# Performance work log

Measured on AMD Instinct MI355X. Metric: run time of the kernel, lower is better.

## Reference

```python
import jax, jax.numpy as jnp
import numpy as np

HIDDEN = 2048
INNER = 1024
NUM_EXPERTS = 64
TOP_K = 8
T_TOKENS = 512


def setup_inputs() -> dict:
    key = jax.random.key(0)
    k_x, k_gw, k_gb, k_w1, k_w2 = jax.random.split(key, 5)
    x = jax.random.normal(k_x, (T_TOKENS, HIDDEN), dtype=jnp.float32)
    gate_w = jax.random.normal(k_gw, (NUM_EXPERTS, HIDDEN), dtype=jnp.float32) * 0.02
    gate_b = jax.random.normal(k_gb, (NUM_EXPERTS,), dtype=jnp.float32) * 0.02
    # fc1: fused gate+up, [E, 2*INNER, HIDDEN]; fc2: down, [E, HIDDEN, INNER]
    w1 = jax.random.normal(k_w1, (NUM_EXPERTS, 2 * INNER, HIDDEN), dtype=jnp.float32) * 0.02
    w2 = jax.random.normal(k_w2, (NUM_EXPERTS, HIDDEN, INNER), dtype=jnp.float32) * 0.02
    return {"x": x, "gate_w": gate_w, "gate_b": gate_b, "w1": w1, "w2": w2}


def reference(x, gate_w, gate_b, w1, w2):
    # Router: ReplicatedLinear with bias -> logits [T, E]
    logits = x @ gate_w.T + gate_b
    # FusedMoE default routing: softmax (fp32), top-k, renormalize
    probs = jax.nn.softmax(logits.astype(jnp.float32), axis=-1)
    topk_w, topk_idx = jax.lax.top_k(probs, TOP_K)          # [T, K]
    topk_w = topk_w / jnp.sum(topk_w, axis=-1, keepdims=True)
    T, E = probs.shape
    # Sparse combine weights scattered into a dense [T, E] matrix
    combine = jnp.zeros((T, E), dtype=topk_w.dtype)
    combine = combine.at[jnp.arange(T)[:, None], topk_idx].add(topk_w)
    # Expert MLPs (dense-over-experts reference; combine zeros out unrouted pairs)
    h = jnp.einsum('th,eih->tei', x, w1)                    # [T, E, 2*INNER]
    gate_h, up_h = h[..., :INNER], h[..., INNER:]
    act = jax.nn.gelu(gate_h, approximate=True) * up_h      # gelu_pytorch_tanh
    y = jnp.einsum('tei,ehi->teh', act, w2)                 # [T, E, HIDDEN]
    # Weighted scatter-combine back to tokens
    return jnp.einsum('te,teh->th', combine.astype(x.dtype), y)
```

## Files before the change

### kernel.cpp

```cpp
#include <hip/hip_runtime.h>
#include <hip/hip_bf16.h>

#define HIDDEN 2048
#define INNER  1024
#define NE     64
#define TOPK   8
#define NTOK   512

typedef float f32x4 __attribute__((ext_vector_type(4)));
typedef short bf16x8 __attribute__((ext_vector_type(8)));

static __device__ __forceinline__ unsigned short b16(float f) {
  return __builtin_bit_cast(unsigned short, __float2bfloat16(f));
}
static __device__ __forceinline__ unsigned int pk2(float lo, float hi) {
  return (unsigned)b16(lo) | ((unsigned)b16(hi) << 16);
}

static __device__ __forceinline__ void decode_ce32(int flat, int& c, int& e) {
  int xcd = flat & 7, s = flat >> 3;
  c = s & 31;
  e = ((s >> 5) << 3) | xcd;
}

__global__ __launch_bounds__(256) void gating_kernel(
    const float* __restrict__ x, const float* __restrict__ gw, const float* __restrict__ gb,
    int* __restrict__ ticket, int* __restrict__ counts, int* __restrict__ offsets,
    int* __restrict__ topk_e, float* __restrict__ topk_w,
    int* __restrict__ perm_tok, int* __restrict__ invpos,
    unsigned short* __restrict__ xb) {
  const int t = blockIdx.x;
  const int tid = threadIdx.x;
  const int lane = tid & 63, w = tid >> 6;

  {
    const float4* xi = (const float4*)(x + (size_t)t * HIDDEN);
    float4 v0 = xi[tid * 2], v1 = xi[tid * 2 + 1];
    ushort4 o0, o1;
    o0.x = b16(v0.x); o0.y = b16(v0.y); o0.z = b16(v0.z); o0.w = b16(v0.w);
    o1.x = b16(v1.x); o1.y = b16(v1.y); o1.z = b16(v1.z); o1.w = b16(v1.w);
    ushort4* xo = (ushort4*)(xb + (size_t)t * HIDDEN);
    xo[tid * 2] = o0; xo[tid * 2 + 1] = o1;
  }

  const int e = tid >> 2, seg = tid & 3;
  const f32x4* gr = (const f32x4*)(gw + (size_t)e * HIDDEN);
  const f32x4* xr = (const f32x4*)(x + (size_t)t * HIDDEN);
  float acc = 0.f;
  #pragma unroll 8
  for (int k = 0; k < 128; ++k) {
    int idx = k * 4 + seg;
    f32x4 a = xr[idx], b = gr[idx];
    acc += a.x * b.x + a.y * b.y + a.z * b.z + a.w * b.w;
  }
  acc += __shfl_xor(acc, 1);
  acc += __shfl_xor(acc, 2);
  __shared__ float sP[NE];
  if (seg == 0) sP[e] = acc;
  __syncthreads();

  __shared__ float sW[TOPK];
  __shared__ int   sE[TOPK];
  if (w == 0) {
    float logit = gb[lane] + sP[lane];
    float m = logit;
    #pragma unroll
    for (int off = 32; off; off >>= 1) m = fmaxf(m, __shfl_xor(m, off));
    float p = __expf(logit - m);
    float s = p;
    #pragma unroll
    for (int off = 32; off; off >>= 1) s += __shfl_xor(s, off);
    p /= s;
    float myp = p;
    #pragma unroll
    for (int k = 0; k < TOPK; ++k) {
      float v = myp; int ei = lane;
      #pragma unroll
      for (int off = 32; off; off >>= 1) {
        float v2 = __shfl_xor(v, off); int e2 = __shfl_xor(ei, off);
        if (v2 > v || (v2 == v && e2 < ei)) { v = v2; ei = e2; }
      }
      if (lane == 0) { sW[k] = v; sE[k] = ei; }
      if (lane == ei) myp = -1.0f;
    }
  }
  __syncthreads();
  if (tid < TOPK) {
    float ss = 0.f;
    #pragma unroll
    for (int k = 0; k < TOPK; ++k) ss += sW[k];
    topk_e[t * TOPK + tid] = sE[tid];
    topk_w[t * TOPK + tid] = sW[tid] / ss;
  }

  __threadfence();
  __syncthreads();
  __shared__ int slast;
  if (tid == 0) {
    int old = atomicAdd(ticket, 1);
    slast = (old == (int)gridDim.x - 1);
  }
  __syncthreads();
  if (!slast) return;
  __threadfence();

  __shared__ int hcnt[NE], soff[NE], ccur[NE];
  if (tid < NE) hcnt[tid] = 0;
  __syncthreads();
  for (int i = tid; i < NTOK * TOPK; i += 256) atomicAdd(&hcnt[topk_e[i]], 1);
  __syncthreads();
  if (tid < NE) {
    int c = hcnt[tid];
    int s = c;
    #pragma unroll
    for (int off = 1; off < 64; off <<= 1) {
      int o = __shfl_up(s, off);
      if (tid >= off) s += o;
    }
    soff[tid] = s - c; ccur[tid] = 0;
    counts[tid] = c; offsets[tid] = s - c;
  }
  __syncthreads();
  for (int i = tid; i < NTOK * TOPK; i += 256) {
    int ee = topk_e[i];
    int p = atomicAdd(&ccur[ee], 1);
    int pos = soff[ee] + p;
    perm_tok[pos] = i >> 3;
    invpos[i] = pos;
  }
}

__global__ __launch_bounds__(256, 3) void phase1_kernel(
    const unsigned short* __restrict__ xb, const float* __restrict__ w1,
    const int* __restrict__ offsets, const int* __restrict__ counts,
    const int* __restrict__ perm_tok, unsigned short* __restrict__ act) {
  int c, e;
  decode_ce32(blockIdx.x, c, e);
  const int n_e = counts[e];
  if (n_e == 0) return;
  const int off = offsets[e];
  const int tid = threadIdx.x;
  const int lane = tid & 63, wave = tid >> 6;
  const int u2 = lane >> 4, l15 = lane & 15;
  const int mat = wave >> 1;
  const int wm  = (wave & 1) * 64;

  const int r16 = tid >> 4, l16 = tid & 15;
  const float* wg  = w1 + (size_t)e * (2 * INNER) * HIDDEN;
  const float* rp0 = wg + (size_t)(c * 32 + r16) * HIDDEN;
  const float* rp1 = rp0 + (size_t)16 * HIDDEN;
  const float* rp2 = wg + (size_t)(INNER + c * 32 + r16) * HIDDEN;
  const float* rp3 = rp2 + (size_t)16 * HIDDEN;
  const int bidx0 = r16 * 16 + (((l16 >> 1) ^ (r16 & 7)) << 1) + (l16 & 1);

  const int ar = tid >> 3, as = tid & 7;
  const int sxa = as ^ (ar & 7);

  __shared__ uint4 smem[2][1536];
  __shared__ int stok[128];
  float (*sU)[36] = (float(*)[36])&smem[0][0];

  for (int m0 = 0; m0 < n_e; m0 += 128) {
    __syncthreads();
    if (tid < 128) {
      int idx = m0 + tid;
      stok[tid] = perm_tok[off + (idx < n_e ? idx : n_e - 1)];
    }
    __syncthreads();

    const unsigned short* xr0 = xb + (size_t)stok[ar] * HIDDEN;
    const unsigned short* xr1 = xb + (size_t)stok[ar + 32] * HIDDEN;
    const unsigned short* xr2 = xb + (size_t)stok[ar + 64] * HIDDEN;
    const unsigned short* xr3 = xb + (size_t)stok[ar + 96] * HIDDEN;

    uint4 va0 = *((const uint4*)xr0 + as);
    uint4 va1 = *((const uint4*)xr1 + as);
    uint4 va2 = *((const uint4*)xr2 + as);
    uint4 va3 = *((const uint4*)xr3 + as);
    f32x4 vB0 = *((const f32x4*)rp0 + l16);
    f32x4 vB1 = *((const f32x4*)rp1 + l16);
    f32x4 vB2 = *((const f32x4*)rp2 + l16);
    f32x4 vB3 = *((const f32x4*)rp3 + l16);

    f32x4 acc[4][2];
    #pragma unroll
    for (int i = 0; i < 4; ++i)
      #pragma unroll
      for (int j = 0; j < 2; ++j) acc[i][j] = (f32x4)0.f;

    for (int k0 = 0; k0 < HIDDEN; k0 += 64) {
      const int cur = (k0 >> 6) & 1;
      uint4* A = smem[cur];
      A[ar * 8 + sxa]          = va0;
      A[(ar + 32) * 8 + sxa]   = va1;
      A[(ar + 64) * 8 + sxa]   = va2;
      A[(ar + 96) * 8 + sxa]   = va3;
      {
        uint2* bb = (uint2*)(smem[cur] + 1024);
        bb[bidx0]       = make_uint2(pk2(vB0.x, vB0.y), pk2(vB0.z, vB0.w));
        bb[bidx0 + 256] = make_uint2(pk2(vB1.x, vB1.y), pk2(vB1.z, vB1.w));
        bb[bidx0 + 512] = make_uint2(pk2(vB2.x, vB2.y), pk2(vB2.z, vB2.w));
        bb[bidx0 + 768] = make_uint2(pk2(vB3.x, vB3.y), pk2(vB3.z, vB3.w));
      }
      __syncthreads();
      int k1 = k0 + 64;
      if (k1 < HIDDEN) {
        va0 = *((const uint4*)(xr0 + k1) + as);
        va1 = *((const uint4*)(xr1 + k1) + as);
        va2 = *((const uint4*)(xr2 + k1) + as);
        va3 = *((const uint4*)(xr3 + k1) + as);
        vB0 = *((const f32x4*)(rp0 + k1) + l16);
        vB1 = *((const f32x4*)(rp1 + k1) + l16);
        vB2 = *((const f32x4*)(rp2 + k1) + l16);
        vB3 = *((const f32x4*)(rp3 + k1) + l16);
      }
      const uint4* Bq = smem[cur] + 1024;
      #pragma unroll
      for (int ks = 0; ks < 2; ++ks) {
        const int u = ks * 4 + u2;
        bf16x8 af[4], bfr[2];
        #pragma unroll
        for (int mi = 0; mi < 4; ++mi) {
          int r = wm + mi * 16 + l15;
          af[mi] = __builtin_bit_cast(bf16x8, A[r * 8 + (u ^ (r & 7))]);
        }
        #pragma unroll
        for (int ni = 0; ni < 2; ++ni) {
          int r = mat * 32 + ni * 16 + l15;
          bfr[ni] = __builtin_bit_cast(bf16x8, Bq[r * 8 + (u ^ (r & 7))]);
        }
        #pragma unroll
        for (int mi = 0; mi < 4; ++mi)
          #pragma unroll
          for (int ni = 0; ni < 2; ++ni)
            acc[mi][ni] = __builtin_amdgcn_mfma_f32_16x16x32_bf16(af[mi], bfr[ni], acc[mi][ni], 0, 0, 0);
      }
    }

    __syncthreads();
    if (mat == 1) {
      #pragma unroll
      for (int mi = 0; mi < 4; ++mi)
        #pragma unroll
        for (int ni = 0; ni < 2; ++ni)
          #pragma unroll
          for (int r4 = 0; r4 < 4; ++r4)
            sU[wm + mi * 16 + u2 * 4 + r4][ni * 16 + l15] = acc[mi][ni][r4];
    }
    __syncthreads();
    if (mat == 0) {
      #pragma unroll
      for (int mi = 0; mi < 4; ++mi)
        #pragma unroll
        for (int r4 = 0; r4 < 4; ++r4) {
          int mrow = wm + mi * 16 + u2 * 4 + r4;
          int m = m0 + mrow;
          if (m < n_e) {
            unsigned short* arow = act + (size_t)(off + m) * INNER + c * 32;
            #pragma unroll
            for (int ni = 0; ni < 2; ++ni) {
              int col = ni * 16 + l15;
              float g = acc[mi][ni][r4];
              float uu = sU[mrow][col];
              float ge = g / (1.0f + __expf(-1.5957691216057308f * (g + 0.044715f * g * g * g)));
              arow[col] = b16(ge * uu);
            }
          }
        }
    }
  }
}

__global__ __launch_bounds__(256, 3) void phase2_kernel(
    const unsigned short* __restrict__ act, const float* __restrict__ w2,
    const int* __restrict__ offsets, const int* __restrict__ counts,
    float* __restrict__ ybuf) {
  int c, e;
  decode_ce32(blockIdx.x, c, e);
  const int n_e = counts[e];
  if (n_e == 0) return;
  const int off = offsets[e];
  const int tid = threadIdx.x;
  const int lane = tid & 63, wave = tid >> 6;
  const int u2 = lane >> 4, l15 = lane & 15;
  const int wm = wave * 32;

  const int r16 = tid >> 4, l16 = tid & 15;
  const float* rp0 = w2 + ((size_t)e * HIDDEN + c * 64 + r16) * INNER;
  const float* rp1 = rp0 + (size_t)16 * INNER;
  const float* rp2 = rp0 + (size_t)32 * INNER;
  const float* rp3 = rp0 + (size_t)48 * INNER;
  const int bidx0 = r16 * 16 + (((l16 >> 1) ^ (r16 & 7)) << 1) + (l16 & 1);

  const int ar = tid >> 3, as = tid & 7;
  const int sxa = as ^ (ar & 7);

  __shared__ uint4 smem[2][1536];

  for (int m0 = 0; m0 < n_e; m0 += 128) {
    const unsigned short* a0 = act + (size_t)(off + (m0 + ar      < n_e ? m0 + ar      : n_e - 1)) * INNER;
    const unsigned short* a1 = act + (size_t)(off + (m0 + ar + 32 < n_e ? m0 + ar + 32 : n_e - 1)) * INNER;
    const unsigned short* a2 = act + (size_t)(off + (m0 + ar + 64 < n_e ? m0 + ar + 64 : n_e - 1)) * INNER;
    const unsigned short* a3 = act + (size_t)(off + (m0 + ar + 96 < n_e ? m0 + ar + 96 : n_e - 1)) * INNER;

    uint4 va0 = *((const uint4*)a0 + as);
    uint4 va1 = *((const uint4*)a1 + as);
    uint4 va2 = *((const uint4*)a2 + as);
    uint4 va3 = *((const uint4*)a3 + as);
    f32x4 vB0 = *((const f32x4*)rp0 + l16);
    f32x4 vB1 = *((const f32x4*)rp1 + l16);
    f32x4 vB2 = *((const f32x4*)rp2 + l16);
    f32x4 vB3 = *((const f32x4*)rp3 + l16);

    f32x4 acc[2][4];
    #pragma unroll
    for (int i = 0; i < 2; ++i)
      #pragma unroll
      for (int j = 0; j < 4; ++j) acc[i][j] = (f32x4)0.f;

    for (int k0 = 0; k0 < INNER; k0 += 64) {
      const int cur = (k0 >> 6) & 1;
      uint4* A = smem[cur];
      A[ar * 8 + sxa]          = va0;
      A[(ar + 32) * 8 + sxa]   = va1;
      A[(ar + 64) * 8 + sxa]   = va2;
      A[(ar + 96) * 8 + sxa]   = va3;
      {
        uint2* bb = (uint2*)(smem[cur] + 1024);
        bb[bidx0]       = make_uint2(pk2(vB0.x, vB0.y), pk2(vB0.z, vB0.w));
        bb[bidx0 + 256] = make_uint2(pk2(vB1.x, vB1.y), pk2(vB1.z, vB1.w));
        bb[bidx0 + 512] = make_uint2(pk2(vB2.x, vB2.y), pk2(vB2.z, vB2.w));
        bb[bidx0 + 768] = make_uint2(pk2(vB3.x, vB3.y), pk2(vB3.z, vB3.w));
      }
      __syncthreads();
      int k1 = k0 + 64;
      if (k1 < INNER) {
        va0 = *((const uint4*)(a0 + k1) + as);
        va1 = *((const uint4*)(a1 + k1) + as);
        va2 = *((const uint4*)(a2 + k1) + as);
        va3 = *((const uint4*)(a3 + k1) + as);
        vB0 = *((const f32x4*)(rp0 + k1) + l16);
        vB1 = *((const f32x4*)(rp1 + k1) + l16);
        vB2 = *((const f32x4*)(rp2 + k1) + l16);
        vB3 = *((const f32x4*)(rp3 + k1) + l16);
      }
      const uint4* Bq = smem[cur] + 1024;
      #pragma unroll
      for (int ks = 0; ks < 2; ++ks) {
        const int u = ks * 4 + u2;
        bf16x8 af[2], bfr[4];
        #pragma unroll
        for (int mi = 0; mi < 2; ++mi) {
          int r = wm + mi * 16 + l15;
          af[mi] = __builtin_bit_cast(bf16x8, A[r * 8 + (u ^ (r & 7))]);
        }
        #pragma unroll
        for (int ni = 0; ni < 4; ++ni) {
          int r = ni * 16 + l15;
          bfr[ni] = __builtin_bit_cast(bf16x8, Bq[r * 8 + (u ^ (r & 7))]);
        }
        #pragma unroll
        for (int mi = 0; mi < 2; ++mi)
          #pragma unroll
          for (int ni = 0; ni < 4; ++ni)
            acc[mi][ni] = __builtin_amdgcn_mfma_f32_16x16x32_bf16(af[mi], bfr[ni], acc[mi][ni], 0, 0, 0);
      }
    }

    #pragma unroll
    for (int mi = 0; mi < 2; ++mi)
      #pragma unroll
      for (int r4 = 0; r4 < 4; ++r4) {
        int mrow = wm + mi * 16 + u2 * 4 + r4;
        int m = m0 + mrow;
        if (m < n_e) {
          float* orow = ybuf + (size_t)(off + m) * HIDDEN + c * 64;
          #pragma unroll
          for (int ni = 0; ni < 4; ++ni)
            orow[ni * 16 + l15] = acc[mi][ni][r4];
        }
      }
    __syncthreads();
  }
}

__global__ __launch_bounds__(256) void combine_kernel(const float* __restrict__ ybuf,
                                                      const int* __restrict__ invpos,
                                                      const float* __restrict__ topk_w,
                                                      float* __restrict__ out) {
  int t = blockIdx.x;
  int tid = threadIdx.x;
  int col = tid * 8;
  f32x4 a0 = (f32x4)0.f, a1 = (f32x4)0.f;
  #pragma unroll
  for (int k = 0; k < TOPK; ++k) {
    int p = invpos[t * TOPK + k];
    float w = topk_w[t * TOPK + k];
    const f32x4* yr = (const f32x4*)(ybuf + (size_t)p * HIDDEN + col);
    f32x4 v0 = yr[0], v1 = yr[1];
    a0 += w * v0;
    a1 += w * v1;
  }
  f32x4* o = (f32x4*)(out + (size_t)t * HIDDEN + col);
  o[0] = a0; o[1] = a1;
}

extern "C" void kernel_launch(void* const* d_in, const int* in_sizes, int n_in,
                              void* d_out, int out_size, void* d_ws, size_t ws_size,
                              hipStream_t stream) {
  const float* x  = (const float*)d_in[0];
  const float* gw = (const float*)d_in[1];
  const float* gb = (const float*)d_in[2];
  const float* w1 = (const float*)d_in[3];
  const float* w2 = (const float*)d_in[4];
  float* out = (float*)d_out;

  char* ws = (char*)d_ws;
  int*   ticket   = (int*)(ws + 0x000);
  int*   counts   = (int*)(ws + 0x100);
  int*   offsets  = (int*)(ws + 0x200);
  int*   topk_e   = (int*)(ws + 0x1000);
  float* topk_w   = (float*)(ws + 0x5000);
  int*   perm_tok = (int*)(ws + 0x9000);
  int*   invpos   = (int*)(ws + 0xD000);
  unsigned short* xb  = (unsigned short*)(ws + 0x11000);
  unsigned short* act = (unsigned short*)(ws + 0x220000);
  float* ybuf         = (float*)(ws + 0xA20000);

  hipMemsetAsync(ticket, 0, 0x40, stream);

  gating_kernel<<<NTOK, 256, 0, stream>>>(x, gw, gb, ticket, counts, offsets,
                                          topk_e, topk_w, perm_tok, invpos, xb);
  phase1_kernel<<<2048, 256, 0, stream>>>(xb, w1, offsets, counts, perm_tok, act);
  phase2_kernel<<<2048, 256, 0, stream>>>(act, w2, offsets, counts, ybuf);
  combine_kernel<<<NTOK, 256, 0, stream>>>(ybuf, invpos, topk_w, out);
}
```

Before: 440.7 us.

## Fuse weighted combine into phase2 via atomicAdd scatter to output

Drops the separate combine kernel and the ybuf intermediate. Phase2 now scales each expert output row by its routing weight and atomically adds it into the token's output row, which the gating kernel zeroes beforehand. This removes the 4M-float ybuf write/read and one kernel launch. In exchange it adds fp32 atomic traffic and makes the summation order nondeterministic.

```diff
diff --git a/kernel.cpp b/kernel.cpp
--- a/kernel.cpp
+++ b/kernel.cpp
@@ -27,8 +27,8 @@
     const float* __restrict__ x, const float* __restrict__ gw, const float* __restrict__ gb,
     int* __restrict__ ticket, int* __restrict__ counts, int* __restrict__ offsets,
     int* __restrict__ topk_e, float* __restrict__ topk_w,
-    int* __restrict__ perm_tok, int* __restrict__ invpos,
-    unsigned short* __restrict__ xb) {
+    int* __restrict__ perm_tok, float* __restrict__ perm_wt,
+    unsigned short* __restrict__ xb, float* __restrict__ out) {
   const int t = blockIdx.x;
   const int tid = threadIdx.x;
   const int lane = tid & 63, w = tid >> 6;
@@ -41,6 +41,9 @@
     o1.x = b16(v1.x); o1.y = b16(v1.y); o1.z = b16(v1.z); o1.w = b16(v1.w);
     ushort4* xo = (ushort4*)(xb + (size_t)t * HIDDEN);
     xo[tid * 2] = o0; xo[tid * 2 + 1] = o1;
+    f32x4 z = (f32x4)0.f;
+    f32x4* orow = (f32x4*)(out + (size_t)t * HIDDEN);
+    orow[tid * 2] = z; orow[tid * 2 + 1] = z;
   }
 
   const int e = tid >> 2, seg = tid & 3;
@@ -126,7 +129,7 @@
     int p = atomicAdd(&ccur[ee], 1);
     int pos = soff[ee] + p;
     perm_tok[pos] = i >> 3;
-    invpos[i] = pos;
+    perm_wt[pos] = topk_w[i];
   }
 }
 
@@ -274,7 +277,8 @@
 __global__ __launch_bounds__(256, 3) void phase2_kernel(
     const unsigned short* __restrict__ act, const float* __restrict__ w2,
     const int* __restrict__ offsets, const int* __restrict__ counts,
-    float* __restrict__ ybuf) {
+    const int* __restrict__ perm_tok, const float* __restrict__ perm_wt,
+    float* __restrict__ out) {
   int c, e;
   decode_ce32(blockIdx.x, c, e);
   const int n_e = counts[e];
@@ -296,8 +300,19 @@
   const int sxa = as ^ (ar & 7);
 
   __shared__ uint4 smem[2][1536];
+  __shared__ int   stok[128];
+  __shared__ float swt[128];
 
   for (int m0 = 0; m0 < n_e; m0 += 128) {
+    __syncthreads();
+    if (tid < 128) {
+      int idx = m0 + tid;
+      int cl = idx < n_e ? idx : n_e - 1;
+      stok[tid] = perm_tok[off + cl];
+      swt[tid] = (idx < n_e) ? perm_wt[off + cl] : 0.f;
+    }
+    __syncthreads();
+
     const unsigned short* a0 = act + (size_t)(off + (m0 + ar      < n_e ? m0 + ar      : n_e - 1)) * INNER;
     const unsigned short* a1 = act + (size_t)(off + (m0 + ar + 32 < n_e ? m0 + ar + 32 : n_e - 1)) * INNER;
     const unsigned short* a2 = act + (size_t)(off + (m0 + ar + 64 < n_e ? m0 + ar + 64 : n_e - 1)) * INNER;
@@ -374,35 +389,16 @@
         int mrow = wm + mi * 16 + u2 * 4 + r4;
         int m = m0 + mrow;
         if (m < n_e) {
-          float* orow = ybuf + (size_t)(off + m) * HIDDEN + c * 64;
+          int tok = stok[mrow];
+          float wt = swt[mrow];
+          float* orow = out + (size_t)tok * HIDDEN + c * 64;
           #pragma unroll
           for (int ni = 0; ni < 4; ++ni)
-            orow[ni * 16 + l15] = acc[mi][ni][r4];
-        }
-      }
-    __syncthreads();
-  }
-}
-
-__global__ __launch_bounds__(256) void combine_kernel(const float* __restrict__ ybuf,
-                                                      const int* __restrict__ invpos,
-                                                      const float* __restrict__ topk_w,
-                                                      float* __restrict__ out) {
-  int t = blockIdx.x;
-  int tid = threadIdx.x;
-  int col = tid * 8;
-  f32x4 a0 = (f32x4)0.f, a1 = (f32x4)0.f;
-  #pragma unroll
-  for (int k = 0; k < TOPK; ++k) {
-    int p = invpos[t * TOPK + k];
-    float w = topk_w[t * TOPK + k];
-    const f32x4* yr = (const f32x4*)(ybuf + (size_t)p * HIDDEN + col);
-    f32x4 v0 = yr[0], v1 = yr[1];
-    a0 += w * v0;
-    a1 += w * v1;
-  }
-  f32x4* o = (f32x4*)(out + (size_t)t * HIDDEN + col);
-  o[0] = a0; o[1] = a1;
+            atomicAdd(&orow[ni * 16 + l15], wt * acc[mi][ni][r4]);
+        }
+      }
+    __syncthreads();
+  }
 }
 
 extern "C" void kernel_launch(void* const* d_in, const int* in_sizes, int n_in,
@@ -422,16 +418,14 @@
   int*   topk_e   = (int*)(ws + 0x1000);
   float* topk_w   = (float*)(ws + 0x5000);
   int*   perm_tok = (int*)(ws + 0x9000);
-  int*   invpos   = (int*)(ws + 0xD000);
+  float* perm_wt  = (float*)(ws + 0xD000);
   unsigned short* xb  = (unsigned short*)(ws + 0x11000);
   unsigned short* act = (unsigned short*)(ws + 0x220000);
-  float* ybuf         = (float*)(ws + 0xA20000);
 
   hipMemsetAsync(ticket, 0, 0x40, stream);
 
   gating_kernel<<<NTOK, 256, 0, stream>>>(x, gw, gb, ticket, counts, offsets,
-                                          topk_e, topk_w, perm_tok, invpos, xb);
+                                          topk_e, topk_w, perm_tok, perm_wt, xb, out);
   phase1_kernel<<<2048, 256, 0, stream>>>(xb, w1, offsets, counts, perm_tok, act);
-  phase2_kernel<<<2048, 256, 0, stream>>>(act, w2, offsets, counts, ybuf);
-  combine_kernel<<<NTOK, 256, 0, stream>>>(ybuf, invpos, topk_w, out);
-}
+  phase2_kernel<<<2048, 256, 0, stream>>>(act, w2, offsets, counts, perm_tok, perm_wt, out);
+}
```

Measured after the change: 436.0 us. Within noise of the previous version (-1.1%).
